# Optimization experiments

Hardware: AMD Instinct MI355X
Metric: run time of the kernel (lower is better)

The kernel has to match this reference:

```python
import jax, jax.numpy as jnp
import numpy as np
from jax import lax

B, S, D, H, T = 128, 512, 128, 128, 20


def setup_inputs() -> dict:
    key = jax.random.key(0)
    ks = jax.random.split(key, 16)
    sc = 1.0 / np.sqrt(H)
    u = lambda k, shape: jax.random.uniform(k, shape, jnp.float32, -sc, sc)
    return {
        "inputs": jax.random.normal(ks[0], (B, S, D), jnp.float32),
        "tags": jax.random.randint(ks[1], (B, S), 0, T),
        "mask": jnp.ones((B, S), jnp.bool_),
        "w_ih_f": u(ks[2], (4 * H, D)),
        "w_hh_f": u(ks[3], (4 * H, H)),
        "b_f": u(ks[4], (4 * H,)),
        "w_ih_b": u(ks[5], (4 * H, D)),
        "w_hh_b": u(ks[6], (4 * H, H)),
        "b_b": u(ks[7], (4 * H,)),
        "w_out": u(ks[8], (T, 2 * H)),
        "b_out": u(ks[9], (T,)),
        "start_trans": jax.random.uniform(ks[10], (T,), jnp.float32, -0.1, 0.1),
        "end_trans": jax.random.uniform(ks[11], (T,), jnp.float32, -0.1, 0.1),
        "trans": jax.random.uniform(ks[12], (T, T), jnp.float32, -0.1, 0.1),
    }


def _lstm_dir(x, w_ih, w_hh, b, reverse):
    # x: [B,S,D] -> hidden states [B,S,H]
    xp = jnp.einsum('bsd,gd->bsg', x, w_ih) + b  # precomputed input gates [B,S,4H]
    if reverse:
        xp = xp[:, ::-1]
    h0 = jnp.zeros((x.shape[0], H), x.dtype)
    c0 = jnp.zeros((x.shape[0], H), x.dtype)

    def step(carry, xt):
        h, c = carry
        g = xt + h @ w_hh.T
        i, f, gg, o = jnp.split(g, 4, axis=-1)
        i, f, o = jax.nn.sigmoid(i), jax.nn.sigmoid(f), jax.nn.sigmoid(o)
        c = f * c + i * jnp.tanh(gg)
        h = o * jnp.tanh(c)
        return (h, c), h

    _, hs = lax.scan(step, (h0, c0), xp.transpose(1, 0, 2))
    hs = hs.transpose(1, 0, 2)  # [B,S,H]
    if reverse:
        hs = hs[:, ::-1]
    return hs


def _crf_nll(em, tags, mask, start_trans, end_trans, trans):
    # em: [B,S,T]; torchcrf log-likelihood, reduction='mean', negated
    b, s, t = em.shape
    maskf = mask.astype(em.dtype)
    batch = jnp.arange(b)
    # numerator: score of the gold path
    num = start_trans[tags[:, 0]] + em[batch, 0, tags[:, 0]]
    em_tag = jnp.take_along_axis(em, tags[:, :, None], axis=2)[:, :, 0]  # [B,S]
    trans_tag = trans[tags[:, :-1], tags[:, 1:]]  # [B,S-1]
    num = num + jnp.sum((trans_tag + em_tag[:, 1:]) * maskf[:, 1:], axis=1)
    seq_ends = jnp.sum(mask.astype(jnp.int32), axis=1) - 1
    num = num + end_trans[tags[batch, seq_ends]]
    # denominator: forward algorithm (logsumexp semiring) via scan
    score0 = start_trans[None, :] + em[:, 0]  # [B,T]

    def step(score, inp):
        em_t, m_t = inp
        nxt = jax.nn.logsumexp(score[:, :, None] + trans[None] + em_t[:, None, :], axis=1)
        return jnp.where(m_t[:, None], nxt, score), None

    score, _ = lax.scan(step, score0, (em[:, 1:].transpose(1, 0, 2), mask[:, 1:].T))
    den = jax.nn.logsumexp(score + end_trans[None, :], axis=1)
    return -jnp.mean(num - den)


def reference(inputs, tags, mask, w_ih_f, w_hh_f, b_f, w_ih_b, w_hh_b, b_b,
              w_out, b_out, start_trans, end_trans, trans):
    h_f = _lstm_dir(inputs, w_ih_f, w_hh_f, b_f, reverse=False)
    h_b = _lstm_dir(inputs, w_ih_b, w_hh_b, b_b, reverse=True)
    lstm_out = jnp.concatenate([h_f, h_b], axis=-1)  # [B,S,2H]
    emissions = jnp.einsum('bsh,th->bst', lstm_out, w_out) + b_out  # [B,S,T]
    return _crf_nll(emissions, tags, mask, start_trans, end_trans, trans)
```

## Files before the change

kernel.cpp:

```cpp
#include <hip/hip_runtime.h>
#include <cstdint>
#include <cstddef>

#define DEVINL __device__ __forceinline__

constexpr int Bz = 128, Sl = 512, Dm = 128, Hd = 128, NC = 1024, Tt = 20;
constexpr int Mrows = Bz * Sl;

constexpr size_t OFF_WBF  = 0;
constexpr size_t OFF_HS   = 151261184;
constexpr size_t OFF_EM   = 184815616;
constexpr size_t OFF_PART = 190058496;

constexpr float LOG2E  = 1.4426950408889634f;
constexpr float LOG2E2 = 2.8853900817779268f;

constexpr int XL9 = 76;

DEVINL unsigned short f2bf(float f) {
    uint32_t u = __float_as_uint(f);
    u += 0x7fffu + ((u >> 16) & 1u);
    return (unsigned short)(u >> 16);
}
DEVINL float bf2f(unsigned short h) { return __uint_as_float(((uint32_t)h) << 16); }

DEVINL float rcpf(float x) { return __builtin_amdgcn_rcpf(x); }
DEVINL float exp2f_fast(float x) { return __builtin_amdgcn_exp2f(x); }

DEVINL void barrier_lds_only() {
    __asm__ __volatile__("s_waitcnt lgkmcnt(0)" ::: "memory");
    __builtin_amdgcn_s_barrier();
    __asm__ __volatile__("" ::: "memory");
}

typedef __attribute__((ext_vector_type(8))) __bf16 bf16x8;
typedef __attribute__((ext_vector_type(4))) float f32x4;
typedef _Float16 __attribute__((ext_vector_type(2))) half2_t;
typedef _Float16 __attribute__((ext_vector_type(8))) half8_t;

__global__ __launch_bounds__(256) void wcvt_k(
    const float* __restrict__ wf, const float* __restrict__ wb,
    unsigned short* __restrict__ o)
{
    const int idx = (blockIdx.x * 256 + threadIdx.x) * 4;
    const float* src = (idx < 65536) ? (wf + idx) : (wb + (idx - 65536));
    float4 v = *(const float4*)src;
    ushort4 u; u.x = f2bf(v.x); u.y = f2bf(v.y); u.z = f2bf(v.z); u.w = f2bf(v.w);
    *(ushort4*)(o + idx) = u;
}

__global__ __launch_bounds__(512, 1) void lstm_k(
    const float* __restrict__ X, const unsigned short* __restrict__ wbf,
    const float* __restrict__ b_f, const float* __restrict__ b_b,
    const float* __restrict__ whf, const float* __restrict__ whb,
    unsigned short* __restrict__ hs)
{
    __shared__ __align__(16) unsigned short xl[512 * XL9];
    __shared__ __align__(16) unsigned short Xs[64 * 132];
    __shared__ __align__(16) _Float16 h_buf[2][128];
    const int dir = blockIdx.x >> 7;
    const int b   = blockIdx.x & 127;
    const int tid = threadIdx.x;
    const int lane = tid & 63;
    const int wv   = tid >> 6;
    const int ln   = lane & 15;
    const int qd   = lane >> 4;
    const int u    = wv * 16 + ln;

    const float* wsrc = dir ? whb : whf;
    half8_t wfr[4][4];
    #pragma unroll
    for (int j = 0; j < 4; ++j) {
        const float sc = (j == 2) ? LOG2E2 : LOG2E;
        const float* wrow = wsrc + (size_t)(j * 128 + u) * 128;
        #pragma unroll
        for (int kk = 0; kk < 4; ++kk) {
            float4 v0 = *(const float4*)(wrow + kk * 32 + qd * 8);
            float4 v1 = *(const float4*)(wrow + kk * 32 + qd * 8 + 4);
            half8_t hv;
            hv[0] = (_Float16)(v0.x * sc); hv[1] = (_Float16)(v0.y * sc);
            hv[2] = (_Float16)(v0.z * sc); hv[3] = (_Float16)(v0.w * sc);
            hv[4] = (_Float16)(v1.x * sc); hv[5] = (_Float16)(v1.y * sc);
            hv[6] = (_Float16)(v1.z * sc); hv[7] = (_Float16)(v1.w * sc);
            wfr[j][kk] = hv;
        }
    }

    bf16x8 wih[4][4];
    #pragma unroll
    for (int n = 0; n < 4; ++n)
        #pragma unroll
        for (int k = 0; k < 4; ++k)
            wih[n][k] = *(const bf16x8*)&wbf[((size_t)(dir * 512 + wv * 64 + n * 16 + ln)) * 128
                                            + k * 32 + qd * 8];
    const float* bsrc = dir ? b_b : b_f;
    float bvn[4];
    #pragma unroll
    for (int n = 0; n < 4; ++n) bvn[n] = bsrc[wv * 64 + n * 16 + ln];
    const float scw = ((wv >> 1) == 2) ? LOG2E2 : LOG2E;

    if (tid < 128) { h_buf[0][tid] = (_Float16)0.f; h_buf[1][tid] = (_Float16)0.f; }
    __syncthreads();

    const float* Xb = X + (size_t)b * 512 * 128;
    const int colc = (tid & 31) * 4, rowb = tid >> 5;

    unsigned short* hptr = hs + (size_t)dir * Mrows * 128 + (size_t)b * Sl * 128 + u
                              + (dir ? (size_t)(Sl - 1) * 128 : 0);
    const int hstep = dir ? -128 : 128;

    float c = 0.f;
    const f32x4 zc = {0.f, 0.f, 0.f, 0.f};

    const int r0 = (0 * 128 + u) * XL9;
    const int r1 = (1 * 128 + u) * XL9;
    const int r2 = (2 * 128 + u) * XL9;
    const int r3 = (3 * 128 + u) * XL9;

    float4 xrg[4];
    {
        const int tlo = dir ? 448 : 0;
        #pragma unroll
        for (int r = 0; r < 4; ++r)
            xrg[r] = *(const float4*)&Xb[(size_t)(tlo + rowb + r * 16) * 128 + colc];
    }

    for (int ch = 0; ch < 8; ++ch) {
        #pragma unroll
        for (int r = 0; r < 4; ++r) {
            const int row = rowb + r * 16;
            float4 av = xrg[r];
            ushort4 au; au.x = f2bf(av.x); au.y = f2bf(av.y); au.z = f2bf(av.z); au.w = f2bf(av.w);
            *(ushort4*)&Xs[row * 132 + colc] = au;
        }
        barrier_lds_only();

        {
            f32x4 acc[4][4];
            #pragma unroll
            for (int k = 0; k < 4; ++k) {
                const int kb = k * 32 + qd * 8;
                bf16x8 af[4];
                #pragma unroll
                for (int m = 0; m < 4; ++m)
                    af[m] = *(const bf16x8*)&Xs[(m * 16 + ln) * 132 + kb];
                #pragma unroll
                for (int m = 0; m < 4; ++m)
                    #pragma unroll
                    for (int n = 0; n < 4; ++n)
                        acc[m][n] = (k == 0)
                            ? __builtin_amdgcn_mfma_f32_16x16x32_bf16(af[m], wih[n][0], zc, 0, 0, 0)
                            : __builtin_amdgcn_mfma_f32_16x16x32_bf16(af[m], wih[n][k], acc[m][n], 0, 0, 0);
            }
            #pragma unroll
            for (int m = 0; m < 4; ++m)
                #pragma unroll
                for (int n = 0; n < 4; ++n) {
                    const int gg = wv * 64 + n * 16 + ln;
                    ushort4 o;
                    o.x = f2bf((acc[m][n][0] + bvn[n]) * scw);
                    o.y = f2bf((acc[m][n][1] + bvn[n]) * scw);
                    o.z = f2bf((acc[m][n][2] + bvn[n]) * scw);
                    o.w = f2bf((acc[m][n][3] + bvn[n]) * scw);
                    *(ushort4*)&xl[gg * XL9 + m * 16 + qd * 4] = o;
                }
        }

        if (ch < 7) {
            const int tlo = dir ? (448 - 64 * (ch + 1)) : (64 * (ch + 1));
            #pragma unroll
            for (int r = 0; r < 4; ++r)
                xrg[r] = *(const float4*)&Xb[(size_t)(tlo + rowb + r * 16) * 128 + colc];
        }
        barrier_lds_only();

        const int tt0 = dir ? 60 : 0;
        ushort4 cur0, cur1, cur2, cur3;
        {
            ushort4 q0 = *(const ushort4*)&xl[r0 + tt0];
            ushort4 q1 = *(const ushort4*)&xl[r1 + tt0];
            ushort4 q2 = *(const ushort4*)&xl[r2 + tt0];
            ushort4 q3 = *(const ushort4*)&xl[r3 + tt0];
            cur0 = dir ? ushort4{q0.w, q0.z, q0.y, q0.x} : q0;
            cur1 = dir ? ushort4{q1.w, q1.z, q1.y, q1.x} : q1;
            cur2 = dir ? ushort4{q2.w, q2.z, q2.y, q2.x} : q2;
            cur3 = dir ? ushort4{q3.w, q3.z, q3.y, q3.x} : q3;
        }

        for (int gi = 0; gi < 16; ++gi) {
            #pragma unroll
            for (int j = 0; j < 4; ++j) {
                __asm__ __volatile__(""
                    : "+v"(wfr[j][0]), "+v"(wfr[j][1]), "+v"(wfr[j][2]), "+v"(wfr[j][3]));
            }
            int ttn = dir ? (56 - gi * 4) : (gi * 4 + 4);
            if (ttn < 0) ttn = 0;
            ushort4 n0 = *(const ushort4*)&xl[r0 + ttn];
            ushort4 n1 = *(const ushort4*)&xl[r1 + ttn];
            ushort4 n2 = *(const ushort4*)&xl[r2 + ttn];
            ushort4 n3 = *(const ushort4*)&xl[r3 + ttn];

            #pragma unroll
            for (int s = 0; s < 4; ++s) {
                const int p = s & 1;
                const half8_t* hb = (const half8_t*)&h_buf[p][0];
                half8_t a0 = hb[qd];
                half8_t a1 = hb[4 + qd];
                half8_t a2 = hb[8 + qd];
                half8_t a3 = hb[12 + qd];

                f32x4 ac0, ac1, ac2, ac3;
                ac0 = __builtin_amdgcn_mfma_f32_16x16x32_f16(a0, wfr[0][0], zc, 0, 0, 0);
                ac1 = __builtin_amdgcn_mfma_f32_16x16x32_f16(a0, wfr[1][0], zc, 0, 0, 0);
                ac2 = __builtin_amdgcn_mfma_f32_16x16x32_f16(a0, wfr[2][0], zc, 0, 0, 0);
                ac3 = __builtin_amdgcn_mfma_f32_16x16x32_f16(a0, wfr[3][0], zc, 0, 0, 0);
                ac0 = __builtin_amdgcn_mfma_f32_16x16x32_f16(a1, wfr[0][1], ac0, 0, 0, 0);
                ac1 = __builtin_amdgcn_mfma_f32_16x16x32_f16(a1, wfr[1][1], ac1, 0, 0, 0);
                ac2 = __builtin_amdgcn_mfma_f32_16x16x32_f16(a1, wfr[2][1], ac2, 0, 0, 0);
                ac3 = __builtin_amdgcn_mfma_f32_16x16x32_f16(a1, wfr[3][1], ac3, 0, 0, 0);
                ac0 = __builtin_amdgcn_mfma_f32_16x16x32_f16(a2, wfr[0][2], ac0, 0, 0, 0);
                ac1 = __builtin_amdgcn_mfma_f32_16x16x32_f16(a2, wfr[1][2], ac1, 0, 0, 0);
                ac2 = __builtin_amdgcn_mfma_f32_16x16x32_f16(a2, wfr[2][2], ac2, 0, 0, 0);
                ac3 = __builtin_amdgcn_mfma_f32_16x16x32_f16(a2, wfr[3][2], ac3, 0, 0, 0);
                ac0 = __builtin_amdgcn_mfma_f32_16x16x32_f16(a3, wfr[0][3], ac0, 0, 0, 0);
                ac1 = __builtin_amdgcn_mfma_f32_16x16x32_f16(a3, wfr[1][3], ac1, 0, 0, 0);
                ac2 = __builtin_amdgcn_mfma_f32_16x16x32_f16(a3, wfr[2][3], ac2, 0, 0, 0);
                ac3 = __builtin_amdgcn_mfma_f32_16x16x32_f16(a3, wfr[3][3], ac3, 0, 0, 0);

                const unsigned short xb0 = (s == 0) ? cur0.x : (s == 1) ? cur0.y : (s == 2) ? cur0.z : cur0.w;
                const unsigned short xb1 = (s == 0) ? cur1.x : (s == 1) ? cur1.y : (s == 2) ? cur1.z : cur1.w;
                const unsigned short xb2 = (s == 0) ? cur2.x : (s == 1) ? cur2.y : (s == 2) ? cur2.z : cur2.w;
                const unsigned short xb3 = (s == 0) ? cur3.x : (s == 1) ? cur3.y : (s == 2) ? cur3.z : cur3.w;

                float t0 = ac0[0] + bf2f(xb0);
                float t1 = ac1[0] + bf2f(xb1);
                float t2 = ac2[0] + bf2f(xb2);
                float t3 = ac3[0] + bf2f(xb3);

                float gi_ = rcpf(1.f + exp2f_fast(-t0));
                float gf_ = rcpf(1.f + exp2f_fast(-t1));
                float gg_ = 2.f * rcpf(1.f + exp2f_fast(-t2)) - 1.f;
                float go_ = rcpf(1.f + exp2f_fast(-t3));
                c = fmaf(gf_, c, gi_ * gg_);
                float th = 1.f - 2.f * rcpf(1.f + exp2f_fast(LOG2E2 * c));
                float h = go_ * th;

                if (qd == 0) {
                    _Float16 hh = (_Float16)h;
                    h_buf[1 - p][u] = hh;
                    unsigned short hbits; __builtin_memcpy(&hbits, &hh, 2);
                    *hptr = hbits;
                }
                hptr += hstep;
                barrier_lds_only();
            }
            cur0 = dir ? ushort4{n0.w, n0.z, n0.y, n0.x} : n0;
            cur1 = dir ? ushort4{n1.w, n1.z, n1.y, n1.x} : n1;
            cur2 = dir ? ushort4{n2.w, n2.z, n2.y, n2.x} : n2;
            cur3 = dir ? ushort4{n3.w, n3.z, n3.y, n3.x} : n3;
        }
    }
}

__global__ __launch_bounds__(320, 1) void emis_k(
    const unsigned short* __restrict__ hs, const float* __restrict__ wout,
    const float* __restrict__ bout, float* __restrict__ em)
{
    __shared__ __align__(16) half2_t wlds[20 * 128];
    const int b  = blockIdx.x >> 2;
    const int qt = blockIdx.x & 3;
    const int tid = threadIdx.x;

    #pragma unroll
    for (int k = 0; k < 8; ++k) {
        int i = tid + k * 320;
        wlds[i] = half2_t{(_Float16)wout[2 * i], (_Float16)wout[2 * i + 1]};
    }
    __syncthreads();

    const int tag  = tid % 20;
    const int copy = tid / 20;
    half2_t wreg[128];
    {
        const uint4* wl4 = (const uint4*)&wlds[tag * 128];
        #pragma unroll
        for (int k = 0; k < 32; ++k) {
            uint4 v = wl4[k];
            __builtin_memcpy(&wreg[4 * k], &v, 16);
        }
    }
    const float bo = bout[tag];
    const unsigned short* hf_base = hs + (size_t)b * Sl * 128;
    const unsigned short* hb_base = hs + (size_t)Mrows * 128 + (size_t)b * Sl * 128;

    #pragma unroll
    for (int i = 0; i < 8; ++i) {
        const int t = qt * 128 + copy + 16 * i;
        const uint4* hf4 = (const uint4*)(hf_base + (size_t)t * 128);
        const uint4* hb4 = (const uint4*)(hb_base + (size_t)t * 128);
        float a0 = bo, a1 = 0.f, a2 = 0.f, a3 = 0.f;
        #pragma unroll
        for (int k = 0; k < 16; ++k) {
            uint4 v = hf4[k];
            half2_t h2[4]; __builtin_memcpy(h2, &v, 16);
            a0 = __builtin_amdgcn_fdot2(wreg[4 * k + 0], h2[0], a0, false);
            a1 = __builtin_amdgcn_fdot2(wreg[4 * k + 1], h2[1], a1, false);
            a2 = __builtin_amdgcn_fdot2(wreg[4 * k + 2], h2[2], a2, false);
            a3 = __builtin_amdgcn_fdot2(wreg[4 * k + 3], h2[3], a3, false);
        }
        #pragma unroll
        for (int k = 0; k < 16; ++k) {
            uint4 v = hb4[k];
            half2_t h2[4]; __builtin_memcpy(h2, &v, 16);
            a0 = __builtin_amdgcn_fdot2(wreg[64 + 4 * k + 0], h2[0], a0, false);
            a1 = __builtin_amdgcn_fdot2(wreg[64 + 4 * k + 1], h2[1], a1, false);
            a2 = __builtin_amdgcn_fdot2(wreg[64 + 4 * k + 2], h2[2], a2, false);
            a3 = __builtin_amdgcn_fdot2(wreg[64 + 4 * k + 3], h2[3], a3, false);
        }
        em[((size_t)b * Sl + t) * Tt + tag] = (a0 + a1) + (a2 + a3);
    }
}

__global__ __launch_bounds__(64) void crf_k(
    const float* __restrict__ em, const int* __restrict__ tags,
    const float* __restrict__ st, const float* __restrict__ et,
    const float* __restrict__ trans, float* __restrict__ part)
{
    const int b = blockIdx.x, lane = threadIdx.x;
    const float* emb = em + (size_t)b * Sl * Tt;
    const int* tg = tags + (size_t)b * Sl;

    float nacc = 0.f;
    for (int t = 1 + lane; t < Sl; t += 64) {
        int tp = tg[t - 1], tc = tg[t];
        nacc += trans[tp * Tt + tc] + emb[t * Tt + tc];
    }
    #pragma unroll
    for (int off = 32; off; off >>= 1) nacc += __shfl_down(nacc, off);

    float Etr[20];
    #pragma unroll
    for (int i = 0; i < 20; ++i)
        Etr[i] = (lane < 20) ? __expf(trans[i * Tt + lane]) : 0.f;

    float C = 0.f;
    float p = (lane < 20) ? __expf(st[lane] + emb[lane]) : 0.f;

    float evr[8];
    #pragma unroll
    for (int s = 0; s < 8; ++s) {
        int tt = 1 + s; tt = tt < Sl ? tt : Sl - 1;
        evr[s] = (lane < 20) ? emb[(size_t)tt * Tt + lane] : 0.f;
    }

    for (int t0 = 1; t0 < Sl; t0 += 8) {
        #pragma unroll
        for (int s = 0; s < 8; ++s) {
            const int t = t0 + s;
            if (t < Sl) {
                float ev = evr[s];
                int tf = t + 8; tf = tf < Sl ? tf : Sl - 1;
                evr[s] = (lane < 20) ? emb[(size_t)tf * Tt + lane] : 0.f;

                float q0 = 0.f, q1 = 0.f, q2 = 0.f, q3 = 0.f;
                #pragma unroll
                for (int i = 0; i < 20; i += 4) {
                    q0 = fmaf(__int_as_float(__builtin_amdgcn_readlane(__float_as_int(p), i + 0)), Etr[i + 0], q0);
                    q1 = fmaf(__int_as_float(__builtin_amdgcn_readlane(__float_as_int(p), i + 1)), Etr[i + 1], q1);
                    q2 = fmaf(__int_as_float(__builtin_amdgcn_readlane(__float_as_int(p), i + 2)), Etr[i + 2], q2);
                    q3 = fmaf(__int_as_float(__builtin_amdgcn_readlane(__float_as_int(p), i + 3)), Etr[i + 3], q3);
                }
                p = ((q0 + q1) + (q2 + q3)) * __expf(ev);
                if ((s & 3) == 3) {
                    float S0 = 0.f, S1 = 0.f, S2 = 0.f, S3 = 0.f;
                    #pragma unroll
                    for (int i = 0; i < 20; i += 4) {
                        S0 += __int_as_float(__builtin_amdgcn_readlane(__float_as_int(p), i + 0));
                        S1 += __int_as_float(__builtin_amdgcn_readlane(__float_as_int(p), i + 1));
                        S2 += __int_as_float(__builtin_amdgcn_readlane(__float_as_int(p), i + 2));
                        S3 += __int_as_float(__builtin_amdgcn_readlane(__float_as_int(p), i + 3));
                    }
                    float Ssum = (S0 + S1) + (S2 + S3);
                    C += __logf(Ssum);
                    p *= rcpf(Ssum);
                }
            }
        }
    }
    float f = (lane < 20) ? p * __expf(et[lane]) : 0.f;
    float S0 = 0.f, S1 = 0.f, S2 = 0.f, S3 = 0.f;
    #pragma unroll
    for (int i = 0; i < 20; i += 4) {
        S0 += __int_as_float(__builtin_amdgcn_readlane(__float_as_int(f), i + 0));
        S1 += __int_as_float(__builtin_amdgcn_readlane(__float_as_int(f), i + 1));
        S2 += __int_as_float(__builtin_amdgcn_readlane(__float_as_int(f), i + 2));
        S3 += __int_as_float(__builtin_amdgcn_readlane(__float_as_int(f), i + 3));
    }
    float den = C + __logf((S0 + S1) + (S2 + S3));
    if (lane == 0)
        part[b] = nacc + st[tg[0]] + emb[tg[0]] + et[tg[Sl - 1]] - den;
}

__global__ void fin_k(const float* __restrict__ part, float* __restrict__ out) {
    int l = threadIdx.x;
    float v = part[l] + part[l + 64];
    #pragma unroll
    for (int off = 32; off; off >>= 1) v += __shfl_xor(v, off);
    if (l == 0) out[0] = -v * (1.f / 128.f);
}

extern "C" void kernel_launch(void* const* d_in, const int* in_sizes, int n_in,
                              void* d_out, int out_size, void* d_ws, size_t ws_size,
                              hipStream_t stream) {
    const float* x      = (const float*)d_in[0];
    const int*   tags   = (const int*)d_in[1];
    const float* w_ih_f = (const float*)d_in[3];
    const float* w_hh_f = (const float*)d_in[4];
    const float* b_f    = (const float*)d_in[5];
    const float* w_ih_b = (const float*)d_in[6];
    const float* w_hh_b = (const float*)d_in[7];
    const float* b_b    = (const float*)d_in[8];
    const float* w_out  = (const float*)d_in[9];
    const float* b_out  = (const float*)d_in[10];
    const float* st     = (const float*)d_in[11];
    const float* et     = (const float*)d_in[12];
    const float* trans  = (const float*)d_in[13];
    float* out = (float*)d_out;

    char* ws = (char*)d_ws;
    unsigned short* wbf  = (unsigned short*)(ws + OFF_WBF);
    unsigned short* hs   = (unsigned short*)(ws + OFF_HS);
    float*          em   = (float*)(ws + OFF_EM);
    float*          part = (float*)(ws + OFF_PART);

    wcvt_k<<<128, 256, 0, stream>>>(w_ih_f, w_ih_b, wbf);
    lstm_k<<<256, 512, 0, stream>>>(x, wbf, b_f, b_b, w_hh_f, w_hh_b, hs);
    emis_k<<<Bz * 4, 320, 0, stream>>>(hs, w_out, b_out, em);
    crf_k<<<Bz, 64, 0, stream>>>(em, tags, st, et, trans, part);
    fin_k<<<1, 64, 0, stream>>>(part, out);
}
```

Measured before the change: 470.9 us.

## Fuse emission projection into CRF kernel and fold weight conversion into LSTM

Removes the separate bf16 weight-conversion kernel by converting w_ih to bf16 inside the LSTM kernel's register load. Merges the emission kernel and the CRF forward kernel into one 640-thread block per batch row that keeps emissions in LDS. This cuts two launches and the global round trip of the emissions tensor. In exchange, emission work runs on 128 blocks instead of 512, and the serial CRF runs on one wave while the rest of the block idles.

```diff
diff --git a/kernel.cpp b/kernel.cpp
--- a/kernel.cpp
+++ b/kernel.cpp
@@ -7,9 +7,7 @@
 constexpr int Bz = 128, Sl = 512, Dm = 128, Hd = 128, NC = 1024, Tt = 20;
 constexpr int Mrows = Bz * Sl;
 
-constexpr size_t OFF_WBF  = 0;
 constexpr size_t OFF_HS   = 151261184;
-constexpr size_t OFF_EM   = 184815616;
 constexpr size_t OFF_PART = 190058496;
 
 constexpr float LOG2E  = 1.4426950408889634f;
@@ -38,19 +36,8 @@
 typedef _Float16 __attribute__((ext_vector_type(2))) half2_t;
 typedef _Float16 __attribute__((ext_vector_type(8))) half8_t;
 
-__global__ __launch_bounds__(256) void wcvt_k(
-    const float* __restrict__ wf, const float* __restrict__ wb,
-    unsigned short* __restrict__ o)
-{
-    const int idx = (blockIdx.x * 256 + threadIdx.x) * 4;
-    const float* src = (idx < 65536) ? (wf + idx) : (wb + (idx - 65536));
-    float4 v = *(const float4*)src;
-    ushort4 u; u.x = f2bf(v.x); u.y = f2bf(v.y); u.z = f2bf(v.z); u.w = f2bf(v.w);
-    *(ushort4*)(o + idx) = u;
-}
-
 __global__ __launch_bounds__(512, 1) void lstm_k(
-    const float* __restrict__ X, const unsigned short* __restrict__ wbf,
+    const float* __restrict__ X, const float* __restrict__ wihf, const float* __restrict__ wihb,
     const float* __restrict__ b_f, const float* __restrict__ b_b,
     const float* __restrict__ whf, const float* __restrict__ whb,
     unsigned short* __restrict__ hs)
@@ -86,13 +73,21 @@
         }
     }
 
+    const float* wisrc = dir ? wihb : wihf;
     bf16x8 wih[4][4];
     #pragma unroll
     for (int n = 0; n < 4; ++n)
         #pragma unroll
-        for (int k = 0; k < 4; ++k)
-            wih[n][k] = *(const bf16x8*)&wbf[((size_t)(dir * 512 + wv * 64 + n * 16 + ln)) * 128
-                                            + k * 32 + qd * 8];
+        for (int k = 0; k < 4; ++k) {
+            const float* wr = wisrc + (size_t)(wv * 64 + n * 16 + ln) * 128 + k * 32 + qd * 8;
+            float4 v0 = *(const float4*)wr;
+            float4 v1 = *(const float4*)(wr + 4);
+            unsigned short us[8];
+            us[0] = f2bf(v0.x); us[1] = f2bf(v0.y); us[2] = f2bf(v0.z); us[3] = f2bf(v0.w);
+            us[4] = f2bf(v1.x); us[5] = f2bf(v1.y); us[6] = f2bf(v1.z); us[7] = f2bf(v1.w);
+            bf16x8 tmp; __builtin_memcpy(&tmp, us, 16);
+            wih[n][k] = tmp;
+        }
     const float* bsrc = dir ? b_b : b_f;
     float bvn[4];
     #pragma unroll
@@ -262,18 +257,20 @@
     }
 }
 
-__global__ __launch_bounds__(320, 1) void emis_k(
+__global__ __launch_bounds__(640, 1) void crfem_k(
     const unsigned short* __restrict__ hs, const float* __restrict__ wout,
-    const float* __restrict__ bout, float* __restrict__ em)
+    const float* __restrict__ bout, const int* __restrict__ tags,
+    const float* __restrict__ st, const float* __restrict__ et,
+    const float* __restrict__ trans, float* __restrict__ part)
 {
     __shared__ __align__(16) half2_t wlds[20 * 128];
-    const int b  = blockIdx.x >> 2;
-    const int qt = blockIdx.x & 3;
+    __shared__ __align__(16) float em_lds[512 * 20];
+    const int b   = blockIdx.x;
     const int tid = threadIdx.x;
 
     #pragma unroll
-    for (int k = 0; k < 8; ++k) {
-        int i = tid + k * 320;
+    for (int k = 0; k < 4; ++k) {
+        int i = tid + k * 640;
         wlds[i] = half2_t{(_Float16)wout[2 * i], (_Float16)wout[2 * i + 1]};
     }
     __syncthreads();
@@ -294,8 +291,8 @@
     const unsigned short* hb_base = hs + (size_t)Mrows * 128 + (size_t)b * Sl * 128;
 
     #pragma unroll
-    for (int i = 0; i < 8; ++i) {
-        const int t = qt * 128 + copy + 16 * i;
+    for (int i = 0; i < 16; ++i) {
+        const int t = copy + 32 * i;
         const uint4* hf4 = (const uint4*)(hf_base + (size_t)t * 128);
         const uint4* hb4 = (const uint4*)(hb_base + (size_t)t * 128);
         float a0 = bo, a1 = 0.f, a2 = 0.f, a3 = 0.f;
@@ -317,88 +314,85 @@
             a2 = __builtin_amdgcn_fdot2(wreg[64 + 4 * k + 2], h2[2], a2, false);
             a3 = __builtin_amdgcn_fdot2(wreg[64 + 4 * k + 3], h2[3], a3, false);
         }
-        em[((size_t)b * Sl + t) * Tt + tag] = (a0 + a1) + (a2 + a3);
-    }
-}
-
-__global__ __launch_bounds__(64) void crf_k(
-    const float* __restrict__ em, const int* __restrict__ tags,
-    const float* __restrict__ st, const float* __restrict__ et,
-    const float* __restrict__ trans, float* __restrict__ part)
-{
-    const int b = blockIdx.x, lane = threadIdx.x;
-    const float* emb = em + (size_t)b * Sl * Tt;
-    const int* tg = tags + (size_t)b * Sl;
-
-    float nacc = 0.f;
-    for (int t = 1 + lane; t < Sl; t += 64) {
-        int tp = tg[t - 1], tc = tg[t];
-        nacc += trans[tp * Tt + tc] + emb[t * Tt + tc];
-    }
-    #pragma unroll
-    for (int off = 32; off; off >>= 1) nacc += __shfl_down(nacc, off);
-
-    float Etr[20];
-    #pragma unroll
-    for (int i = 0; i < 20; ++i)
-        Etr[i] = (lane < 20) ? __expf(trans[i * Tt + lane]) : 0.f;
-
-    float C = 0.f;
-    float p = (lane < 20) ? __expf(st[lane] + emb[lane]) : 0.f;
-
-    float evr[8];
-    #pragma unroll
-    for (int s = 0; s < 8; ++s) {
-        int tt = 1 + s; tt = tt < Sl ? tt : Sl - 1;
-        evr[s] = (lane < 20) ? emb[(size_t)tt * Tt + lane] : 0.f;
-    }
-
-    for (int t0 = 1; t0 < Sl; t0 += 8) {
+        em_lds[t * Tt + tag] = (a0 + a1) + (a2 + a3);
+    }
+    __syncthreads();
+
+    if (tid < 64) {
+        const int lane = tid;
+        const float* emb = em_lds;
+        const int* tg = tags + (size_t)b * Sl;
+
+        float nacc = 0.f;
+        for (int t = 1 + lane; t < Sl; t += 64) {
+            int tp = tg[t - 1], tc = tg[t];
+            nacc += trans[tp * Tt + tc] + emb[t * Tt + tc];
+        }
+        #pragma unroll
+        for (int off = 32; off; off >>= 1) nacc += __shfl_down(nacc, off);
+
+        float Etr[20];
+        #pragma unroll
+        for (int i = 0; i < 20; ++i)
+            Etr[i] = (lane < 20) ? __expf(trans[i * Tt + lane]) : 0.f;
+
+        float C = 0.f;
+        float p = (lane < 20) ? __expf(st[lane] + emb[lane]) : 0.f;
+
+        float evr[8];
         #pragma unroll
         for (int s = 0; s < 8; ++s) {
-            const int t = t0 + s;
-            if (t < Sl) {
-                float ev = evr[s];
-                int tf = t + 8; tf = tf < Sl ? tf : Sl - 1;
-                evr[s] = (lane < 20) ? emb[(size_t)tf * Tt + lane] : 0.f;
-
-                float q0 = 0.f, q1 = 0.f, q2 = 0.f, q3 = 0.f;
-                #pragma unroll
-                for (int i = 0; i < 20; i += 4) {
-                    q0 = fmaf(__int_as_float(__builtin_amdgcn_readlane(__float_as_int(p), i + 0)), Etr[i + 0], q0);
-                    q1 = fmaf(__int_as_float(__builtin_amdgcn_readlane(__float_as_int(p), i + 1)), Etr[i + 1], q1);
-                    q2 = fmaf(__int_as_float(__builtin_amdgcn_readlane(__float_as_int(p), i + 2)), Etr[i + 2], q2);
-                    q3 = fmaf(__int_as_float(__builtin_amdgcn_readlane(__float_as_int(p), i + 3)), Etr[i + 3], q3);
-                }
-                p = ((q0 + q1) + (q2 + q3)) * __expf(ev);
-                if ((s & 3) == 3) {
-                    float S0 = 0.f, S1 = 0.f, S2 = 0.f, S3 = 0.f;
+            int tt = 1 + s; tt = tt < Sl ? tt : Sl - 1;
+            evr[s] = (lane < 20) ? emb[(size_t)tt * Tt + lane] : 0.f;
+        }
+
+        for (int t0 = 1; t0 < Sl; t0 += 8) {
+            #pragma unroll
+            for (int s = 0; s < 8; ++s) {
+                const int t = t0 + s;
+                if (t < Sl) {
+                    float ev = evr[s];
+                    int tf = t + 8; tf = tf < Sl ? tf : Sl - 1;
+                    evr[s] = (lane < 20) ? emb[(size_t)tf * Tt + lane] : 0.f;
+
+                    float q0 = 0.f, q1 = 0.f, q2 = 0.f, q3 = 0.f;
                     #pragma unroll
                     for (int i = 0; i < 20; i += 4) {
-                        S0 += __int_as_float(__builtin_amdgcn_readlane(__float_as_int(p), i + 0));
-                        S1 += __int_as_float(__builtin_amdgcn_readlane(__float_as_int(p), i + 1));
-                        S2 += __int_as_float(__builtin_amdgcn_readlane(__float_as_int(p), i + 2));
-                        S3 += __int_as_float(__builtin_amdgcn_readlane(__float_as_int(p), i + 3));
+                        q0 = fmaf(__int_as_float(__builtin_amdgcn_readlane(__float_as_int(p), i + 0)), Etr[i + 0], q0);
+                        q1 = fmaf(__int_as_float(__builtin_amdgcn_readlane(__float_as_int(p), i + 1)), Etr[i + 1], q1);
+                        q2 = fmaf(__int_as_float(__builtin_amdgcn_readlane(__float_as_int(p), i + 2)), Etr[i + 2], q2);
+                        q3 = fmaf(__int_as_float(__builtin_amdgcn_readlane(__float_as_int(p), i + 3)), Etr[i + 3], q3);
                     }
-                    float Ssum = (S0 + S1) + (S2 + S3);
-                    C += __logf(Ssum);
-                    p *= rcpf(Ssum);
+                    p = ((q0 + q1) + (q2 + q3)) * __expf(ev);
+                    if ((s & 3) == 3) {
+                        float S0 = 0.f, S1 = 0.f, S2 = 0.f, S3 = 0.f;
+                        #pragma unroll
+                        for (int i = 0; i < 20; i += 4) {
+                            S0 += __int_as_float(__builtin_amdgcn_readlane(__float_as_int(p), i + 0));
+                            S1 += __int_as_float(__builtin_amdgcn_readlane(__float_as_int(p), i + 1));
+                            S2 += __int_as_float(__builtin_amdgcn_readlane(__float_as_int(p), i + 2));
+                            S3 += __int_as_float(__builtin_amdgcn_readlane(__float_as_int(p), i + 3));
+                        }
+                        float Ssum = (S0 + S1) + (S2 + S3);
+                        C += __logf(Ssum);
+                        p *= rcpf(Ssum);
+                    }
                 }
             }
         }
-    }
-    float f = (lane < 20) ? p * __expf(et[lane]) : 0.f;
-    float S0 = 0.f, S1 = 0.f, S2 = 0.f, S3 = 0.f;
-    #pragma unroll
-    for (int i = 0; i < 20; i += 4) {
-        S0 += __int_as_float(__builtin_amdgcn_readlane(__float_as_int(f), i + 0));
-        S1 += __int_as_float(__builtin_amdgcn_readlane(__float_as_int(f), i + 1));
-        S2 += __int_as_float(__builtin_amdgcn_readlane(__float_as_int(f), i + 2));
-        S3 += __int_as_float(__builtin_amdgcn_readlane(__float_as_int(f), i + 3));
-    }
-    float den = C + __logf((S0 + S1) + (S2 + S3));
-    if (lane == 0)
-        part[b] = nacc + st[tg[0]] + emb[tg[0]] + et[tg[Sl - 1]] - den;
+        float f = (lane < 20) ? p * __expf(et[lane]) : 0.f;
+        float S0 = 0.f, S1 = 0.f, S2 = 0.f, S3 = 0.f;
+        #pragma unroll
+        for (int i = 0; i < 20; i += 4) {
+            S0 += __int_as_float(__builtin_amdgcn_readlane(__float_as_int(f), i + 0));
+            S1 += __int_as_float(__builtin_amdgcn_readlane(__float_as_int(f), i + 1));
+            S2 += __int_as_float(__builtin_amdgcn_readlane(__float_as_int(f), i + 2));
+            S3 += __int_as_float(__builtin_amdgcn_readlane(__float_as_int(f), i + 3));
+        }
+        float den = C + __logf((S0 + S1) + (S2 + S3));
+        if (lane == 0)
+            part[b] = nacc + st[tg[0]] + emb[tg[0]] + et[tg[Sl - 1]] - den;
+    }
 }
 
 __global__ void fin_k(const float* __restrict__ part, float* __restrict__ out) {
@@ -428,14 +422,10 @@
     float* out = (float*)d_out;
 
     char* ws = (char*)d_ws;
-    unsigned short* wbf  = (unsigned short*)(ws + OFF_WBF);
     unsigned short* hs   = (unsigned short*)(ws + OFF_HS);
-    float*          em   = (float*)(ws + OFF_EM);
     float*          part = (float*)(ws + OFF_PART);
 
-    wcvt_k<<<128, 256, 0, stream>>>(w_ih_f, w_ih_b, wbf);
-    lstm_k<<<256, 512, 0, stream>>>(x, wbf, b_f, b_b, w_hh_f, w_hh_b, hs);
-    emis_k<<<Bz * 4, 320, 0, stream>>>(hs, w_out, b_out, em);
-    crf_k<<<Bz, 64, 0, stream>>>(em, tags, st, et, trans, part);
+    lstm_k<<<256, 512, 0, stream>>>(x, w_ih_f, w_ih_b, b_f, b_b, w_hh_f, w_hh_b, hs);
+    crfem_k<<<Bz, 640, 0, stream>>>(hs, w_out, b_out, tags, st, et, trans, part);
     fin_k<<<1, 64, 0, stream>>>(part, out);
 }
```

Measured after the change: 490.7 us. +4.2%, slower.
